# Kernel tuning notes

Measured on AMD Instinct MI355X. Metric: run time of the kernel, lower is better.

Reference implementation:

```python
import jax, jax.numpy as jnp
import numpy as np

B, S, E, H, FF = 4, 2048, 512, 8, 2048
DH = E // H
EPS = 1e-6


def setup_inputs() -> dict:
    key = jax.random.key(0)
    ks = jax.random.split(key, 16)
    sc = lambda fan_in: 1.0 / np.sqrt(fan_in)
    inp = {
        "x": jax.random.normal(ks[0], (B, S, E), dtype=jnp.float32),
        "src_mask": jnp.ones((B, 1, 1, S), dtype=jnp.int32),
        # attention projections, stored [in, out]
        "wq": jax.random.uniform(ks[1], (E, E), minval=-sc(E), maxval=sc(E)),
        "bq": jnp.zeros((E,), jnp.float32),
        "wk": jax.random.uniform(ks[2], (E, E), minval=-sc(E), maxval=sc(E)),
        "bk": jnp.zeros((E,), jnp.float32),
        "wv": jax.random.uniform(ks[3], (E, E), minval=-sc(E), maxval=sc(E)),
        "bv": jnp.zeros((E,), jnp.float32),
        "wo": jax.random.uniform(ks[4], (E, E), minval=-sc(E), maxval=sc(E)),
        "bo": jnp.zeros((E,), jnp.float32),
        # feed-forward
        "w1": jax.random.uniform(ks[5], (E, FF), minval=-sc(E), maxval=sc(E)),
        "b1": jnp.zeros((FF,), jnp.float32),
        "w2": jax.random.uniform(ks[6], (FF, E), minval=-sc(FF), maxval=sc(FF)),
        "b2": jnp.zeros((E,), jnp.float32),
        # addNormLayer scalar params (alpha init 1, bias init 0)
        "alpha1": jnp.ones((1,), jnp.float32),
        "beta1": jnp.zeros((1,), jnp.float32),
        "alpha2": jnp.ones((1,), jnp.float32),
        "beta2": jnp.zeros((1,), jnp.float32),
    }
    return inp


def _norm(x, alpha, beta):
    # matches torch: mean + unbiased std (ddof=1), eps added to std
    mean = jnp.mean(x, axis=-1, keepdims=True)
    std = jnp.std(x, axis=-1, keepdims=True, ddof=1)
    return alpha * (x - mean) / (std + EPS) + beta


def reference(x, src_mask, wq, bq, wk, bk, wv, bv, wo, bo,
              w1, b1, w2, b2, alpha1, beta1, alpha2, beta2):
    # --- residual 1: pre-norm self-attention ---
    n = _norm(x, alpha1, beta1)  # [B,S,E]
    q = (n @ wq + bq).reshape(B, S, H, DH).transpose(0, 2, 1, 3)  # [B,H,S,DH]
    k = (n @ wk + bk).reshape(B, S, H, DH).transpose(0, 2, 1, 3)
    v = (n @ wv + bv).reshape(B, S, H, DH).transpose(0, 2, 1, 3)
    scores = jnp.einsum('bhqd,bhkd->bhqk', q, k) / np.sqrt(DH)  # [B,H,S,S]
    scores = jnp.where(src_mask == 0, -1e9, scores)
    attn = jax.nn.softmax(scores, axis=-1)
    ctx = jnp.einsum('bhqk,bhkd->bhqd', attn, v)  # [B,H,S,DH]
    ctx = ctx.transpose(0, 2, 1, 3).reshape(B, S, E)
    x = x + (ctx @ wo + bo)
    # --- residual 2: pre-norm FFN ---
    n2 = _norm(x, alpha2, beta2)
    ff = jax.nn.relu(n2 @ w1 + b1) @ w2 + b2
    return x + ff
```

## Files before the change

### kernel.cpp

```cpp
#include <hip/hip_runtime.h>
#include <type_traits>

typedef __bf16 bfrag __attribute__((ext_vector_type(8)));
typedef float f32x4 __attribute__((ext_vector_type(4)));
typedef float f32x16 __attribute__((ext_vector_type(16)));
typedef unsigned short us8 __attribute__((ext_vector_type(8)));
typedef unsigned int u32x2 __attribute__((ext_vector_type(2)));
typedef unsigned int u32x4 __attribute__((ext_vector_type(4)));

__device__ __forceinline__ float bf2f(unsigned short s) {
  unsigned u = ((unsigned)s) << 16;
  float f;
  __builtin_memcpy(&f, &u, 4);
  return f;
}
__device__ __forceinline__ unsigned short f2bf(float f) {
  unsigned u;
  __builtin_memcpy(&u, &f, 4);
  u += 0x7fffu + ((u >> 16) & 1u);
  return (unsigned short)(u >> 16);
}
__device__ __forceinline__ float rdf(const void* p, size_t i, int isf) {
  return isf ? ((const float*)p)[i] : bf2f(((const unsigned short*)p)[i]);
}
__device__ __forceinline__ void gld16(const unsigned short* g, unsigned short* l) {
  __builtin_amdgcn_global_load_lds(
      (const __attribute__((address_space(1))) unsigned int*)g,
      (__attribute__((address_space(3))) unsigned int*)l, 16, 0, 0);
}
__device__ __forceinline__ unsigned cvtpk_bf16(float a, float b) {
  unsigned d;
  asm("v_cvt_pk_bf16_f32 %0, %1, %2" : "=v"(d) : "v"(a), "v"(b));
  return d;
}

template <int XMODE>
__device__ void norm_unit(const void* xin, const void* alpha, const void* beta,
                          unsigned short* out, int isf, int u) {
  constexpr int E = 512;
  int xf = XMODE ? 1 : isf;
  int tid = threadIdx.x;
  int wave = tid >> 6, lane = tid & 63;
  size_t tok = (size_t)u * 4 + wave;
  float v[8];
  if (xf) {
    const float* xp = (const float*)xin + tok * E + lane * 8;
    float4 a0 = *(const float4*)xp;
    float4 a1 = *(const float4*)(xp + 4);
    v[0] = a0.x; v[1] = a0.y; v[2] = a0.z; v[3] = a0.w;
    v[4] = a1.x; v[5] = a1.y; v[6] = a1.z; v[7] = a1.w;
  } else {
    us8 uu = *(const us8*)((const unsigned short*)xin + tok * E + lane * 8);
#pragma unroll
    for (int j = 0; j < 8; j++) v[j] = bf2f(uu[j]);
  }
  float s = 0.f, sq = 0.f;
#pragma unroll
  for (int j = 0; j < 8; j++) { s += v[j]; sq += v[j] * v[j]; }
#pragma unroll
  for (int off = 1; off < 64; off <<= 1) {
    s += __shfl_xor(s, off, 64);
    sq += __shfl_xor(sq, off, 64);
  }
  float mean = s * (1.0f / 512.0f);
  float var = fmaxf((sq - 512.0f * mean * mean) * (1.0f / 511.0f), 0.0f);
  float inv = rdf(alpha, 0, isf) / (sqrtf(var) + 1e-6f);
  float be = rdf(beta, 0, isf);
  us8 ov;
#pragma unroll
  for (int j = 0; j < 8; j++) ov[j] = f2bf((v[j] - mean) * inv + be);
  *(us8*)(out + tok * E + lane * 8) = ov;
}

__global__ __launch_bounds__(256) void setup_k(
    const unsigned short* __restrict__ x16,
    const void* wq, const void* wk, const void* wv, const void* wo,
    const void* w1, const void* w2,
    unsigned short* wqkvT, unsigned short* woT,
    unsigned short* w1T, unsigned short* w2T,
    const void* bq, const void* bk, const void* bv, const void* bo,
    const void* b1, const void* b2, float* __restrict__ bcat,
    const void* alpha1, const void* beta1, unsigned short* __restrict__ n1,
    int* __restrict__ flag) {
  __shared__ unsigned short tile[32][33];
  __shared__ int s_cnt;
  int tid = threadIdx.x;
  int bid = blockIdx.x;
  if (tid == 0) s_cnt = 0;
  __syncthreads();
  {
    int c = 0;
    for (int i = tid; i < 4096; i += 256) {
      unsigned short s = x16[2 * i];
      int e = (s >> 7) & 0xFF;
      if (e > 0xC2 || (e != 0 && e < 0x3D)) c++;
    }
    atomicAdd(&s_cnt, c);
  }
  __syncthreads();
  const int isf = (s_cnt > 256) ? 1 : 0;
  if (bid == 0 && tid == 0) flag[0] = isf;

  if (bid >= 3090) {
    norm_unit<0>(x16, alpha1, beta1, n1, isf, bid - 3090);
    return;
  }
  if (bid >= 3072) {
    int i = (bid - 3072) * 256 + tid;
    if (i < 4608) {
      float v;
      if (i < 512) v = rdf(bq, i, isf);
      else if (i < 1024) v = rdf(bk, i - 512, isf);
      else if (i < 1536) v = rdf(bv, i - 1024, isf);
      else if (i < 2048) v = rdf(bo, i - 1536, isf);
      else if (i < 4096) v = rdf(b1, i - 2048, isf);
      else v = rdf(b2, i - 4096, isf);
      bcat[i] = v;
    }
    return;
  }
  const void* W;
  unsigned short* Wt;
  int K, N, t;
  if (bid < 1024) {
    K = 512; N = 512; t = bid & 255;
    if (bid < 256) { W = wq; Wt = wqkvT; }
    else if (bid < 512) { W = wk; Wt = wqkvT + 262144; }
    else if (bid < 768) { W = wv; Wt = wqkvT + 524288; }
    else { W = wo; Wt = woT; }
  } else if (bid < 2048) {
    W = w1; Wt = w1T; K = 512; N = 2048; t = bid - 1024;
  } else {
    W = w2; Wt = w2T; K = 2048; N = 512; t = bid - 2048;
  }
  int nx = N >> 5;
  int n0 = (t % nx) * 32, k0 = (t / nx) * 32;
#pragma unroll
  for (int i = 0; i < 4; i++) {
    int e = tid + i * 256;
    int r = e >> 5, c = e & 31;
    tile[r][c] = f2bf(rdf(W, (size_t)(k0 + r) * N + n0 + c, isf));
  }
  __syncthreads();
#pragma unroll
  for (int i = 0; i < 4; i++) {
    int e = tid + i * 256;
    int r = e >> 5, c = e & 31;
    Wt[(size_t)(n0 + r) * K + k0 + c] = tile[c][r];
  }
}

__global__ __launch_bounds__(256) void vtrans_k(
    const unsigned short* __restrict__ qkb, unsigned short* __restrict__ vbt) {
  __shared__ unsigned short tile[32][33];
  int tid = threadIdx.x;
  int u = blockIdx.x;
  int s0 = (u & 63) * 32;
  int d0 = ((u >> 6) & 1) * 32;
  int bh = u >> 7, b = bh >> 3, h = bh & 7;
#pragma unroll
  for (int i = 0; i < 4; i++) {
    int e = tid + i * 256;
    int r = e >> 5, c = e & 31;
    tile[r][c] = qkb[((size_t)b * 2048 + s0 + r) * 1536 + 1024 + h * 64 + d0 + c];
  }
  __syncthreads();
#pragma unroll
  for (int i = 0; i < 4; i++) {
    int e = tid + i * 256;
    int r = e >> 5, c = e & 31;
    vbt[((size_t)bh * 64 + d0 + r) * 2048 + s0 + c] = tile[c][r];
  }
}

__global__ __launch_bounds__(256) void norm2_k(
    const void* __restrict__ xin, const void* __restrict__ alpha,
    const void* __restrict__ beta, unsigned short* __restrict__ out,
    const int* __restrict__ flag) {
  norm_unit<1>(xin, alpha, beta, out, flag[0], blockIdx.x);
}

template <int TN, int RES, int OUTM, int RELU>
__global__ __launch_bounds__(256, 3) void gemm2_k(
    const unsigned short* __restrict__ A,
    const unsigned short* __restrict__ Bt,
    const float* __restrict__ bias,
    const void* __restrict__ res,
    void* __restrict__ outp,
    int N, int K, const int* __restrict__ flag) {
  constexpr int MT = (TN == 128) ? 4 : 2;
  constexpr int BROWS = TN / 4;
  __shared__ alignas(16) unsigned short As[128 * 64];
  __shared__ alignas(16) unsigned short Bs[TN * 64];
  int isf = flag[0];
  int outf32 = (OUTM == 1) || (OUTM == 2 && isf);
  int tid = threadIdx.x;
  int wave = tid >> 6, lane = tid & 63;
  int quad = lane >> 4, l16 = lane & 15, l7 = l16 & 7;
  int wm = (TN == 128) ? (wave >> 1) : wave;
  int wn = (TN == 128) ? (wave & 1) : 0;
  size_t m0 = (size_t)blockIdx.x * 128;
  size_t n0 = (size_t)blockIdx.y * TN;

  int lrow = lane >> 3;
  int gcol = 8 * ((lane & 7) ^ lrow);

  const unsigned short* ag = A + (m0 + wave * 32 + lrow) * K + gcol;
  const unsigned short* bg = Bt + (n0 + wave * BROWS + lrow) * K + gcol;
  unsigned short* asl = &As[(wave * 32) * 64];
  unsigned short* bsl = &Bs[(wave * BROWS) * 64];

  f32x4 acc[MT][4];
#pragma unroll
  for (int i = 0; i < MT; i++)
#pragma unroll
    for (int j = 0; j < 4; j++) acc[i][j] = {0.f, 0.f, 0.f, 0.f};

  for (int k0 = 0; k0 < K; k0 += 64) {
    __syncthreads();
#pragma unroll
    for (int c = 0; c < 4; c++)
      gld16(ag + (size_t)(8 * c) * K + k0, asl + (8 * c) * 64);
#pragma unroll
    for (int c = 0; c < BROWS / 8; c++)
      gld16(bg + (size_t)(8 * c) * K + k0, bsl + (8 * c) * 64);
    __syncthreads();
#pragma unroll
    for (int ko = 0; ko < 2; ko++) {
      int slot = ((4 * ko + quad) ^ l7) * 8;
      bfrag af[MT], bf[4];
#pragma unroll
      for (int i = 0; i < MT; i++)
        af[i] = *(const bfrag*)&As[(wm * (MT * 16) + i * 16 + l16) * 64 + slot];
#pragma unroll
      for (int j = 0; j < 4; j++)
        bf[j] = *(const bfrag*)&Bs[(wn * 64 + j * 16 + l16) * 64 + slot];
#pragma unroll
      for (int i = 0; i < MT; i++)
#pragma unroll
        for (int j = 0; j < 4; j++)
          acc[i][j] = __builtin_amdgcn_mfma_f32_16x16x32_bf16(af[i], bf[j], acc[i][j], 0, 0, 0);
    }
  }
#pragma unroll
  for (int j = 0; j < 4; j++) {
    size_t n = n0 + wn * 64 + j * 16 + l16;
    float bv = bias[n];
#pragma unroll
    for (int i = 0; i < MT; i++) {
#pragma unroll
      for (int r = 0; r < 4; r++) {
        size_t m = m0 + wm * (MT * 16) + i * 16 + quad * 4 + r;
        float vv = acc[i][j][r] + bv;
        if (RELU) vv = fmaxf(vv, 0.0f);
        if (RES == 1) vv += rdf(res, m * N + n, isf);
        else if (RES == 2) vv += ((const float*)res)[m * N + n];
        if (outf32) ((float*)outp)[m * N + n] = vv;
        else ((unsigned short*)outp)[m * N + n] = f2bf(vv);
      }
    }
  }
}

__global__ __launch_bounds__(256, 2) void attn_k(
    const unsigned short* __restrict__ qkb,
    const unsigned short* __restrict__ vbt,
    const int* __restrict__ mask,
    unsigned short* __restrict__ ctx) {
  constexpr int S = 2048;
  __shared__ alignas(16) unsigned short Kt[2][2][64 * 64];
  __shared__ alignas(16) unsigned short Vt[2][2][64 * 64];
  __shared__ alignas(16) float mskf[S];
  __shared__ float linv[128];
  __shared__ int s_all;
  int tid = threadIdx.x, wave = tid >> 6, lane = tid & 63;
  int l32 = lane & 31, hi = lane >> 5;

  int lin = blockIdx.x;
  int work = (lin & 7) * 64 + (lin >> 3);
  int bh = work >> 4;
  int q0 = (work & 15) * 128;
  int b = bh >> 3, h = bh & 7;
  size_t rowbase = (size_t)b * S;
  const float SC = 0.18033688f;

  bfrag qf[4];
  {
    const unsigned short* qp =
        qkb + (rowbase + q0 + wave * 32 + l32) * 1536 + h * 64 + hi * 8;
#pragma unroll
    for (int ds = 0; ds < 4; ds++) qf[ds] = *(const bfrag*)(qp + ds * 16);
  }

  int srow_l = lane >> 3;
  int sc = lane & 7;
  int swz = (sc ^ srow_l) * 8;
  const unsigned short* kgb = qkb + 512 + h * 64;
  const unsigned short* vgb = vbt + (size_t)bh * 64 * S;

  const unsigned short* kp[2][2];
  const unsigned short* vp[2][2];
#pragma unroll
  for (int hh = 0; hh < 2; hh++)
#pragma unroll
    for (int i = 0; i < 2; i++) {
      int r = wave * 16 + i * 8 + srow_l;
      kp[hh][i] = kgb + (rowbase + hh * 64 + r) * 1536 + swz;
      vp[hh][i] = vgb + (size_t)r * S + hh * 64 + swz;
    }

  auto STAGE = [&](int buf) {
#pragma unroll
    for (int hh = 0; hh < 2; hh++)
#pragma unroll
      for (int i = 0; i < 2; i++) {
        gld16(kp[hh][i], &Kt[buf][hh][(wave * 16 + i * 8) * 64]);
        kp[hh][i] += 128 * 1536;
        gld16(vp[hh][i], &Vt[buf][hh][(wave * 16 + i * 8) * 64]);
        vp[hh][i] += 128;
      }
  };

  f32x16 o[2];
#pragma unroll
  for (int i = 0; i < 16; i++) { o[0][i] = 0.f; o[1][i] = 0.f; }
  f32x16 z16;
#pragma unroll
  for (int i = 0; i < 16; i++) z16[i] = 0.f;
  float l_i = 0.f;

  STAGE(0);
  if (tid == 0) s_all = 1;
  __syncthreads();
  {
    int ok = 1;
    for (int i = tid; i < S; i += 256) {
      int mv = mask[rowbase + i];
      ok &= (mv != 0);
      mskf[i] = mv ? 0.0f : -1e5f;
    }
    atomicAnd(&s_all, ok);
  }
  __syncthreads();
  int am = s_all;

  auto BODY = [&](auto amc) {
    constexpr bool AM = decltype(amc)::value;
    for (int it = 0; it < S / 128; it++) {
      int kt = it * 128;
      int cur = it & 1;
      if (it + 1 < S / 128) STAGE(cur ^ 1);

      f32x16 pacc0[2], pacc1[2];
      unsigned pb0[16], pb1[16];

#pragma unroll
      for (int hh = 0; hh < 2; hh++) {
        f32x16* pa = hh ? pacc1 : pacc0;
#pragma unroll
        for (int t = 0; t < 2; t++) {
          int r = t * 32 + l32;
#pragma unroll
          for (int ds = 0; ds < 4; ds++) {
            int phys = ((2 * ds + hi) ^ (l32 & 7)) * 8;
            bfrag kf = *(const bfrag*)&Kt[cur][hh][r * 64 + phys];
            pa[t] = __builtin_amdgcn_mfma_f32_32x32x16_bf16(
                kf, qf[ds], ds == 0 ? z16 : pa[t], 0, 0, 0);
          }
        }
      }

#pragma unroll
      for (int hh = 0; hh < 2; hh++) {
        const f32x16* pacc = hh ? pacc1 : pacc0;
        unsigned* pb = hh ? pb1 : pb0;
#pragma unroll
        for (int t = 0; t < 2; t++) {
#pragma unroll
          for (int g = 0; g < 4; g++) {
            float p0, p1, p2, p3;
            if constexpr (AM) {
              p0 = __builtin_amdgcn_exp2f(pacc[t][g * 4 + 0] * SC);
              p1 = __builtin_amdgcn_exp2f(pacc[t][g * 4 + 1] * SC);
              p2 = __builtin_amdgcn_exp2f(pacc[t][g * 4 + 2] * SC);
              p3 = __builtin_amdgcn_exp2f(pacc[t][g * 4 + 3] * SC);
            } else {
              float4 m4 = *(const float4*)&mskf[kt + hh * 64 + t * 32 + g * 8 + hi * 4];
              p0 = __builtin_amdgcn_exp2f(fmaf(pacc[t][g * 4 + 0], SC, m4.x));
              p1 = __builtin_amdgcn_exp2f(fmaf(pacc[t][g * 4 + 1], SC, m4.y));
              p2 = __builtin_amdgcn_exp2f(fmaf(pacc[t][g * 4 + 2], SC, m4.z));
              p3 = __builtin_amdgcn_exp2f(fmaf(pacc[t][g * 4 + 3], SC, m4.w));
            }
            l_i += (p0 + p1) + (p2 + p3);
            pb[t * 8 + g * 2] = cvtpk_bf16(p0, p1);
            pb[t * 8 + g * 2 + 1] = cvtpk_bf16(p2, p3);
          }
        }
#pragma unroll
        for (int ks = 0; ks < 4; ks++) {
          int t = ks >> 1, e = ks & 1;
          u32x2 sA = __builtin_amdgcn_permlane32_swap(
              pb[t * 8 + 4 * e + 0], pb[t * 8 + 4 * e + 2], false, false);
          u32x2 sB = __builtin_amdgcn_permlane32_swap(
              pb[t * 8 + 4 * e + 1], pb[t * 8 + 4 * e + 3], false, false);
          u32x4 pw = {sA.x, sB.x, sA.y, sB.y};
          bfrag pf = __builtin_bit_cast(bfrag, pw);
#pragma unroll
          for (int dt = 0; dt < 2; dt++) {
            int r = dt * 32 + l32;
            int phys = ((2 * ks + hi) ^ (l32 & 7)) * 8;
            bfrag vf = *(const bfrag*)&Vt[cur][hh][r * 64 + phys];
            o[dt] = __builtin_amdgcn_mfma_f32_32x32x16_bf16(pf, vf, o[dt], 0, 0, 0);
          }
        }
      }

      __builtin_amdgcn_sched_group_barrier(0x020, 8, 0);
#pragma unroll
      for (int z = 0; z < 16; z++) {
        __builtin_amdgcn_sched_group_barrier(0x100, 2, 0);
        __builtin_amdgcn_sched_group_barrier(0x008, 2, 0);
        __builtin_amdgcn_sched_group_barrier(0x002, 16, 0);
      }
      __syncthreads();
    }
  };
  if (am) BODY(std::integral_constant<bool, true>{});
  else    BODY(std::integral_constant<bool, false>{});

  {
    unsigned lu = __builtin_bit_cast(unsigned, l_i);
    u32x2 lr = __builtin_amdgcn_permlane32_swap(lu, lu, false, false);
    float l_tot = __builtin_bit_cast(float, lr.x) + __builtin_bit_cast(float, lr.y);
    if (lane < 32) linv[wave * 32 + l32] = 1.0f / fmaxf(l_tot, 1e-30f);
  }
  __syncthreads();
#pragma unroll
  for (int dt = 0; dt < 2; dt++) {
#pragma unroll
    for (int reg = 0; reg < 16; reg++) {
      int ql = (reg & 3) + 8 * (reg >> 2) + 4 * hi;
      size_t qrow = rowbase + q0 + wave * 32 + ql;
      ctx[qrow * 512 + h * 64 + dt * 32 + l32] =
          f2bf(o[dt][reg] * linv[wave * 32 + ql]);
    }
  }
}

extern "C" void kernel_launch(void* const* d_in, const int* in_sizes, int n_in,
                              void* d_out, int out_size, void* d_ws, size_t ws_size,
                              hipStream_t stream) {
  const unsigned short* x = (const unsigned short*)d_in[0];
  const int* mask         = (const int*)d_in[1];
  const void* wq = d_in[2];  const void* bq = d_in[3];
  const void* wk = d_in[4];  const void* bk = d_in[5];
  const void* wv = d_in[6];  const void* bv = d_in[7];
  const void* wo = d_in[8];  const void* bo = d_in[9];
  const void* w1 = d_in[10]; const void* b1 = d_in[11];
  const void* w2 = d_in[12]; const void* b2 = d_in[13];
  const void* alpha1 = d_in[14]; const void* beta1 = d_in[15];
  const void* alpha2 = d_in[16]; const void* beta2 = d_in[17];

  char* ws = (char*)d_ws;
  int* flag            = (int*)(ws + 0);
  unsigned short* wqkvT= (unsigned short*)(ws + 65536);
  unsigned short* woT  = (unsigned short*)(ws + 1638400);
  unsigned short* w1T  = (unsigned short*)(ws + 2162688);
  unsigned short* w2T  = (unsigned short*)(ws + 4259840);
  float*          bcat = (float*)         (ws + 6356992);
  float*          x1   = (float*)         (ws + 6422528);
  unsigned short* n1   = (unsigned short*)(ws + 23199744);
  unsigned short* qkb  = (unsigned short*)(ws + 31588352);
  unsigned short* vbt  = (unsigned short*)(ws + 56754176);
  unsigned short* ff1  = qkb;

  dim3 blk(256);

  setup_k<<<5138, blk, 0, stream>>>(x, wq, wk, wv, wo, w1, w2,
                                    wqkvT, woT, w1T, w2T,
                                    bq, bk, bv, bo, b1, b2, bcat,
                                    alpha1, beta1, n1, flag);
  gemm2_k<128, 0, 0, 0><<<dim3(64, 12), blk, 0, stream>>>(n1, wqkvT, bcat, nullptr, qkb, 1536, 512, flag);
  vtrans_k<<<4096, blk, 0, stream>>>(qkb, vbt);
  attn_k<<<512, blk, 0, stream>>>(qkb, vbt, mask, n1);
  gemm2_k<64, 1, 1, 0><<<dim3(64, 8), blk, 0, stream>>>(n1, woT, bcat + 1536, (const void*)x, x1, 512, 512, flag);
  norm2_k<<<2048, blk, 0, stream>>>(x1, alpha2, beta2, n1, flag);
  gemm2_k<128, 0, 0, 1><<<dim3(64, 16), blk, 0, stream>>>(n1, w1T, bcat + 2048, nullptr, ff1, 2048, 512, flag);
  gemm2_k<64, 2, 2, 0><<<dim3(64, 8), blk, 0, stream>>>(ff1, w2T, bcat + 4096, x1, d_out, 512, 2048, flag);
}
```

Before: 272.5 us.

## Split attention key range across two wave groups with in-block merge

The attention kernel now runs 512 threads per block. Two groups of four waves each process half of the key sequence (1024 keys) for the same 128 queries, in 64-key tiles with their own double-buffered K/V shared memory. At the end, the second group writes its partial output and row sums to shared memory (reusing the K buffer), and the first group merges, normalizes and stores. The aim is more waves in flight per CU to hide latency. In exchange it adds a shared-memory merge step, and the hand-written sched_group_barrier interleaving is removed.

```diff
diff --git a/kernel.cpp b/kernel.cpp
--- a/kernel.cpp
+++ b/kernel.cpp
@@ -262,7 +262,7 @@
   }
 }
 
-__global__ __launch_bounds__(256, 2) void attn_k(
+__global__ __launch_bounds__(512, 4) void attn_k(
     const unsigned short* __restrict__ qkb,
     const unsigned short* __restrict__ vbt,
     const int* __restrict__ mask,
@@ -271,9 +271,10 @@
   __shared__ alignas(16) unsigned short Kt[2][2][64 * 64];
   __shared__ alignas(16) unsigned short Vt[2][2][64 * 64];
   __shared__ alignas(16) float mskf[S];
-  __shared__ float linv[128];
+  __shared__ float ml[2][128];
   __shared__ int s_all;
   int tid = threadIdx.x, wave = tid >> 6, lane = tid & 63;
+  int kh = wave >> 2, wv = wave & 3;
   int l32 = lane & 31, hi = lane >> 5;
 
   int lin = blockIdx.x;
@@ -287,7 +288,7 @@
   bfrag qf[4];
   {
     const unsigned short* qp =
-        qkb + (rowbase + q0 + wave * 32 + l32) * 1536 + h * 64 + hi * 8;
+        qkb + (rowbase + q0 + wv * 32 + l32) * 1536 + h * 64 + hi * 8;
 #pragma unroll
     for (int ds = 0; ds < 4; ds++) qf[ds] = *(const bfrag*)(qp + ds * 16);
   }
@@ -298,27 +299,23 @@
   const unsigned short* kgb = qkb + 512 + h * 64;
   const unsigned short* vgb = vbt + (size_t)bh * 64 * S;
 
-  const unsigned short* kp[2][2];
-  const unsigned short* vp[2][2];
-#pragma unroll
-  for (int hh = 0; hh < 2; hh++)
+  const unsigned short* kp[2];
+  const unsigned short* vp[2];
+#pragma unroll
+  for (int i = 0; i < 2; i++) {
+    int r = wv * 16 + i * 8 + srow_l;
+    kp[i] = kgb + (rowbase + kh * 1024 + r) * 1536 + swz;
+    vp[i] = vgb + (size_t)r * S + kh * 1024 + swz;
+  }
+
+  auto STAGE = [&](int buf) {
 #pragma unroll
     for (int i = 0; i < 2; i++) {
-      int r = wave * 16 + i * 8 + srow_l;
-      kp[hh][i] = kgb + (rowbase + hh * 64 + r) * 1536 + swz;
-      vp[hh][i] = vgb + (size_t)r * S + hh * 64 + swz;
-    }
-
-  auto STAGE = [&](int buf) {
-#pragma unroll
-    for (int hh = 0; hh < 2; hh++)
-#pragma unroll
-      for (int i = 0; i < 2; i++) {
-        gld16(kp[hh][i], &Kt[buf][hh][(wave * 16 + i * 8) * 64]);
-        kp[hh][i] += 128 * 1536;
-        gld16(vp[hh][i], &Vt[buf][hh][(wave * 16 + i * 8) * 64]);
-        vp[hh][i] += 128;
-      }
+      gld16(kp[i], &Kt[kh][buf][(wv * 16 + i * 8) * 64]);
+      kp[i] += 64 * 1536;
+      gld16(vp[i], &Vt[kh][buf][(wv * 16 + i * 8) * 64]);
+      vp[i] += 64;
+    }
   };
 
   f32x16 o[2];
@@ -334,7 +331,7 @@
   __syncthreads();
   {
     int ok = 1;
-    for (int i = tid; i < S; i += 256) {
+    for (int i = tid; i < S; i += 512) {
       int mv = mask[rowbase + i];
       ok &= (mv != 0);
       mskf[i] = mv ? 0.0f : -1e5f;
@@ -346,81 +343,64 @@
 
   auto BODY = [&](auto amc) {
     constexpr bool AM = decltype(amc)::value;
-    for (int it = 0; it < S / 128; it++) {
-      int kt = it * 128;
+    for (int it = 0; it < 16; it++) {
       int cur = it & 1;
-      if (it + 1 < S / 128) STAGE(cur ^ 1);
-
-      f32x16 pacc0[2], pacc1[2];
-      unsigned pb0[16], pb1[16];
-
-#pragma unroll
-      for (int hh = 0; hh < 2; hh++) {
-        f32x16* pa = hh ? pacc1 : pacc0;
-#pragma unroll
-        for (int t = 0; t < 2; t++) {
-          int r = t * 32 + l32;
-#pragma unroll
-          for (int ds = 0; ds < 4; ds++) {
-            int phys = ((2 * ds + hi) ^ (l32 & 7)) * 8;
-            bfrag kf = *(const bfrag*)&Kt[cur][hh][r * 64 + phys];
-            pa[t] = __builtin_amdgcn_mfma_f32_32x32x16_bf16(
-                kf, qf[ds], ds == 0 ? z16 : pa[t], 0, 0, 0);
+      if (it + 1 < 16) STAGE(cur ^ 1);
+
+      f32x16 pacc[2];
+#pragma unroll
+      for (int t = 0; t < 2; t++) {
+        int r = t * 32 + l32;
+#pragma unroll
+        for (int ds = 0; ds < 4; ds++) {
+          int phys = ((2 * ds + hi) ^ (l32 & 7)) * 8;
+          bfrag kf = *(const bfrag*)&Kt[kh][cur][r * 64 + phys];
+          pacc[t] = __builtin_amdgcn_mfma_f32_32x32x16_bf16(
+              kf, qf[ds], ds == 0 ? z16 : pacc[t], 0, 0, 0);
+        }
+      }
+
+      unsigned pb[16];
+#pragma unroll
+      for (int t = 0; t < 2; t++) {
+#pragma unroll
+        for (int g = 0; g < 4; g++) {
+          float p0, p1, p2, p3;
+          if constexpr (AM) {
+            p0 = __builtin_amdgcn_exp2f(pacc[t][g * 4 + 0] * SC);
+            p1 = __builtin_amdgcn_exp2f(pacc[t][g * 4 + 1] * SC);
+            p2 = __builtin_amdgcn_exp2f(pacc[t][g * 4 + 2] * SC);
+            p3 = __builtin_amdgcn_exp2f(pacc[t][g * 4 + 3] * SC);
+          } else {
+            float4 m4 =
+                *(const float4*)&mskf[kh * 1024 + it * 64 + t * 32 + g * 8 + hi * 4];
+            p0 = __builtin_amdgcn_exp2f(fmaf(pacc[t][g * 4 + 0], SC, m4.x));
+            p1 = __builtin_amdgcn_exp2f(fmaf(pacc[t][g * 4 + 1], SC, m4.y));
+            p2 = __builtin_amdgcn_exp2f(fmaf(pacc[t][g * 4 + 2], SC, m4.z));
+            p3 = __builtin_amdgcn_exp2f(fmaf(pacc[t][g * 4 + 3], SC, m4.w));
           }
+          l_i += (p0 + p1) + (p2 + p3);
+          pb[t * 8 + g * 2] = cvtpk_bf16(p0, p1);
+          pb[t * 8 + g * 2 + 1] = cvtpk_bf16(p2, p3);
         }
       }
 
 #pragma unroll
-      for (int hh = 0; hh < 2; hh++) {
-        const f32x16* pacc = hh ? pacc1 : pacc0;
-        unsigned* pb = hh ? pb1 : pb0;
-#pragma unroll
-        for (int t = 0; t < 2; t++) {
-#pragma unroll
-          for (int g = 0; g < 4; g++) {
-            float p0, p1, p2, p3;
-            if constexpr (AM) {
-              p0 = __builtin_amdgcn_exp2f(pacc[t][g * 4 + 0] * SC);
-              p1 = __builtin_amdgcn_exp2f(pacc[t][g * 4 + 1] * SC);
-              p2 = __builtin_amdgcn_exp2f(pacc[t][g * 4 + 2] * SC);
-              p3 = __builtin_amdgcn_exp2f(pacc[t][g * 4 + 3] * SC);
-            } else {
-              float4 m4 = *(const float4*)&mskf[kt + hh * 64 + t * 32 + g * 8 + hi * 4];
-              p0 = __builtin_amdgcn_exp2f(fmaf(pacc[t][g * 4 + 0], SC, m4.x));
-              p1 = __builtin_amdgcn_exp2f(fmaf(pacc[t][g * 4 + 1], SC, m4.y));
-              p2 = __builtin_amdgcn_exp2f(fmaf(pacc[t][g * 4 + 2], SC, m4.z));
-              p3 = __builtin_amdgcn_exp2f(fmaf(pacc[t][g * 4 + 3], SC, m4.w));
-            }
-            l_i += (p0 + p1) + (p2 + p3);
-            pb[t * 8 + g * 2] = cvtpk_bf16(p0, p1);
-            pb[t * 8 + g * 2 + 1] = cvtpk_bf16(p2, p3);
-          }
+      for (int ks = 0; ks < 4; ks++) {
+        int t = ks >> 1, e = ks & 1;
+        u32x2 sA = __builtin_amdgcn_permlane32_swap(
+            pb[t * 8 + 4 * e + 0], pb[t * 8 + 4 * e + 2], false, false);
+        u32x2 sB = __builtin_amdgcn_permlane32_swap(
+            pb[t * 8 + 4 * e + 1], pb[t * 8 + 4 * e + 3], false, false);
+        u32x4 pw = {sA.x, sB.x, sA.y, sB.y};
+        bfrag pf = __builtin_bit_cast(bfrag, pw);
+#pragma unroll
+        for (int dt = 0; dt < 2; dt++) {
+          int r = dt * 32 + l32;
+          int phys = ((2 * ks + hi) ^ (l32 & 7)) * 8;
+          bfrag vf = *(const bfrag*)&Vt[kh][cur][r * 64 + phys];
+          o[dt] = __builtin_amdgcn_mfma_f32_32x32x16_bf16(pf, vf, o[dt], 0, 0, 0);
         }
-#pragma unroll
-        for (int ks = 0; ks < 4; ks++) {
-          int t = ks >> 1, e = ks & 1;
-          u32x2 sA = __builtin_amdgcn_permlane32_swap(
-              pb[t * 8 + 4 * e + 0], pb[t * 8 + 4 * e + 2], false, false);
-          u32x2 sB = __builtin_amdgcn_permlane32_swap(
-              pb[t * 8 + 4 * e + 1], pb[t * 8 + 4 * e + 3], false, false);
-          u32x4 pw = {sA.x, sB.x, sA.y, sB.y};
-          bfrag pf = __builtin_bit_cast(bfrag, pw);
-#pragma unroll
-          for (int dt = 0; dt < 2; dt++) {
-            int r = dt * 32 + l32;
-            int phys = ((2 * ks + hi) ^ (l32 & 7)) * 8;
-            bfrag vf = *(const bfrag*)&Vt[cur][hh][r * 64 + phys];
-            o[dt] = __builtin_amdgcn_mfma_f32_32x32x16_bf16(pf, vf, o[dt], 0, 0, 0);
-          }
-        }
-      }
-
-      __builtin_amdgcn_sched_group_barrier(0x020, 8, 0);
-#pragma unroll
-      for (int z = 0; z < 16; z++) {
-        __builtin_amdgcn_sched_group_barrier(0x100, 2, 0);
-        __builtin_amdgcn_sched_group_barrier(0x008, 2, 0);
-        __builtin_amdgcn_sched_group_barrier(0x002, 16, 0);
       }
       __syncthreads();
     }
@@ -432,17 +412,31 @@
     unsigned lu = __builtin_bit_cast(unsigned, l_i);
     u32x2 lr = __builtin_amdgcn_permlane32_swap(lu, lu, false, false);
     float l_tot = __builtin_bit_cast(float, lr.x) + __builtin_bit_cast(float, lr.y);
-    if (lane < 32) linv[wave * 32 + l32] = 1.0f / fmaxf(l_tot, 1e-30f);
-  }
-  __syncthreads();
-#pragma unroll
-  for (int dt = 0; dt < 2; dt++) {
-#pragma unroll
-    for (int reg = 0; reg < 16; reg++) {
-      int ql = (reg & 3) + 8 * (reg >> 2) + 4 * hi;
-      size_t qrow = rowbase + q0 + wave * 32 + ql;
-      ctx[qrow * 512 + h * 64 + dt * 32 + l32] =
-          f2bf(o[dt][reg] * linv[wave * 32 + ql]);
+    if (lane < 32) ml[kh][wv * 32 + l32] = l_tot;
+  }
+  float* mrg = (float*)&Kt[0][0][0];
+  if (kh == 1) {
+#pragma unroll
+    for (int dt = 0; dt < 2; dt++) {
+#pragma unroll
+      for (int reg = 0; reg < 16; reg++) {
+        int ql = (reg & 3) + 8 * (reg >> 2) + 4 * hi;
+        mrg[wv * 2048 + ql * 64 + dt * 32 + l32] = o[dt][reg];
+      }
+    }
+  }
+  __syncthreads();
+  if (kh == 0) {
+#pragma unroll
+    for (int dt = 0; dt < 2; dt++) {
+#pragma unroll
+      for (int reg = 0; reg < 16; reg++) {
+        int ql = (reg & 3) + 8 * (reg >> 2) + 4 * hi;
+        float inv = 1.0f / fmaxf(ml[0][wv * 32 + ql] + ml[1][wv * 32 + ql], 1e-30f);
+        float val = (o[dt][reg] + mrg[wv * 2048 + ql * 64 + dt * 32 + l32]) * inv;
+        size_t qrow = rowbase + q0 + wv * 32 + ql;
+        ctx[qrow * 512 + h * 64 + dt * 32 + l32] = f2bf(val);
+      }
     }
   }
 }
@@ -482,7 +476,7 @@
                                     alpha1, beta1, n1, flag);
   gemm2_k<128, 0, 0, 0><<<dim3(64, 12), blk, 0, stream>>>(n1, wqkvT, bcat, nullptr, qkb, 1536, 512, flag);
   vtrans_k<<<4096, blk, 0, stream>>>(qkb, vbt);
-  attn_k<<<512, blk, 0, stream>>>(qkb, vbt, mask, n1);
+  attn_k<<<512, dim3(512), 0, stream>>>(qkb, vbt, mask, n1);
   gemm2_k<64, 1, 1, 0><<<dim3(64, 8), blk, 0, stream>>>(n1, woT, bcat + 1536, (const void*)x, x1, 512, 512, flag);
   norm2_k<<<2048, blk, 0, stream>>>(x1, alpha2, beta2, n1, flag);
   gemm2_k<128, 0, 0, 1><<<dim3(64, 16), blk, 0, stream>>>(n1, w1T, bcat + 2048, nullptr, ff1, 2048, 512, flag);
```

New measurement: 287.5 us. 5.5% more time.
